# Kernel tuning notes

Hardware: AMD Instinct MI355X
Metric: run time of the kernel (lower is better)

## Reference

```python
import jax, jax.numpy as jnp
import numpy as np

D = 1024
E = 8


def setup_inputs() -> dict:
    key = jax.random.key(0)
    ks = jax.random.split(key, 7)
    s = 1.0 / np.sqrt(D)
    x = jax.random.normal(ks[0], (4, 2048, D), dtype=jnp.float32)
    Wg = jax.random.uniform(ks[1], (D, E), minval=-s, maxval=s, dtype=jnp.float32)
    bg = jax.random.uniform(ks[2], (E,), minval=-s, maxval=s, dtype=jnp.float32)
    W1 = jax.random.uniform(ks[3], (E, D, D), minval=-s, maxval=s, dtype=jnp.float32)
    b1 = jax.random.uniform(ks[4], (E, D), minval=-s, maxval=s, dtype=jnp.float32)
    W2 = jax.random.uniform(ks[5], (E, D, D), minval=-s, maxval=s, dtype=jnp.float32)
    b2 = jax.random.uniform(ks[6], (E, D), minval=-s, maxval=s, dtype=jnp.float32)
    return {"x": x, "Wg": Wg, "bg": bg, "W1": W1, "b1": b1, "W2": W2, "b2": b2}


def reference(x, Wg, bg, W1, b1, W2, b2):
    N, T, d = x.shape
    x_flat = x.reshape(N * T, d)                                  # [NT, D]
    logits = x_flat @ Wg + bg                                     # [NT, E]
    probs = jax.nn.softmax(logits, axis=-1)
    assignments = jnp.argmax(probs, axis=-1)                      # [NT]
    # all-experts MLP (dense, as in the original module)
    h = jnp.einsum('nd,edh->neh', x_flat, W1) + b1[None]          # [NT, E, D]
    h = jax.nn.gelu(h, approximate=False)                         # torch GELU = exact erf
    eo = jnp.einsum('neh,ehd->ned', h, W2) + b2[None]             # [NT, E, D]
    selected = jnp.take_along_axis(eo, assignments[:, None, None], axis=1)[:, 0, :]  # [NT, D]
    w = jnp.take_along_axis(probs, assignments[:, None], axis=1)  # [NT, 1]
    out = (w * selected).reshape(N, T, d)
    return out
```

## Files before the change

kernel.cpp:

```cpp
#include <hip/hip_runtime.h>
#include <cstdint>

#define NT 8192
#define DD 1024
#define NE 8
#define BK 32
#define NKIT (DD / BK)
#define TM 128
#define MAXTILE 72
#define TPX (MAXTILE / 8)

typedef __attribute__((ext_vector_type(8))) _Float16 half8;
typedef __attribute__((ext_vector_type(4))) float f32x4;

__device__ __forceinline__ unsigned short f2h_bits(float f) {
  _Float16 h = (_Float16)f;
  return __builtin_bit_cast(unsigned short, h);
}

#define GLDS16(gp, lp) __builtin_amdgcn_global_load_lds( \
  (__attribute__((address_space(1))) void*)(uintptr_t)(gp), \
  (__attribute__((address_space(3))) void*)(uintptr_t)(lp), 16, 0, 0)

#define WAITCNT_VM4  0xF74
#define WAITCNT_VM0  0xF70

__global__ __launch_bounds__(256) void prep_kernel(
    const float* __restrict__ W1, const float* __restrict__ W2,
    _Float16* __restrict__ W1t, _Float16* __restrict__ W2t,
    const float* __restrict__ x, const float* __restrict__ Wg, const float* __restrict__ bg,
    int* __restrict__ assign, float* __restrict__ wgt, _Float16* __restrict__ xh) {
  __shared__ alignas(16) char smem[32768];
  const int bid = blockIdx.x;
  const int tid = threadIdx.x;
  if (bid < 4096) {
    float (*tile)[65] = (float (*)[65])smem;
    const int z = bid >> 8;
    const float* W = (z < 8 ? W1 : W2) + (size_t)(z & 7) * (DD * DD);
    _Float16* Wt   = (z < 8 ? W1t : W2t) + (size_t)(z & 7) * (DD * DD);
    const int k0 = (bid & 15) * 64, n0 = ((bid >> 4) & 15) * 64;
#pragma unroll
    for (int it = 0; it < 4; ++it) {
      int idx = it * 256 + tid;
      int r = idx >> 4;
      int q = idx & 15;
      float4 v = *(const float4*)(W + (size_t)(k0 + r) * DD + n0 + q * 4);
      tile[r][q * 4 + 0] = v.x; tile[r][q * 4 + 1] = v.y;
      tile[r][q * 4 + 2] = v.z; tile[r][q * 4 + 3] = v.w;
    }
    __syncthreads();
#pragma unroll
    for (int it = 0; it < 4; ++it) {
      int idx = it * 256 + tid;
      int n = idx >> 4;
      int q = idx & 15;
      ushort4 o;
      o.x = f2h_bits(tile[q * 4 + 0][n]);
      o.y = f2h_bits(tile[q * 4 + 1][n]);
      o.z = f2h_bits(tile[q * 4 + 2][n]);
      o.w = f2h_bits(tile[q * 4 + 3][n]);
      *(ushort4*)(Wt + (size_t)(n0 + n) * DD + k0 + q * 4) = o;
    }
  } else {
    float* WgL = (float*)smem;
    const int gb = bid - 4096;
#pragma unroll
    for (int it = 0; it < 8; ++it) {
      int idx = it * 256 + tid;
      float4 v = ((const float4*)Wg)[idx];
      int k = idx >> 1;
      int e0 = (idx & 1) * 4;
      WgL[(e0 + 0) * DD + k] = v.x;
      WgL[(e0 + 1) * DD + k] = v.y;
      WgL[(e0 + 2) * DD + k] = v.z;
      WgL[(e0 + 3) * DD + k] = v.w;
    }
    __syncthreads();
    const int lane = tid & 63, w = tid >> 6;
#pragma unroll
    for (int s = 0; s < 2; ++s) {
      const int t = gb * 8 + w * 2 + s;
      const float4* xr = (const float4*)(x + (size_t)t * DD);
      float4 xv[4];
#pragma unroll
      for (int c = 0; c < 4; ++c) xv[c] = xr[lane + 64 * c];
      ushort4* xo = (ushort4*)(xh + (size_t)t * DD);
#pragma unroll
      for (int c = 0; c < 4; ++c) {
        union { ushort4 u; _Float16 h[4]; } cv;
        cv.h[0] = (_Float16)xv[c].x; cv.h[1] = (_Float16)xv[c].y;
        cv.h[2] = (_Float16)xv[c].z; cv.h[3] = (_Float16)xv[c].w;
        xo[lane + 64 * c] = cv.u;
      }
      float p[NE];
#pragma unroll
      for (int e = 0; e < NE; ++e) {
        float acc = 0.f;
#pragma unroll
        for (int c = 0; c < 4; ++c) {
          float4 wv = *(const float4*)&WgL[e * DD + 4 * lane + 256 * c];
          acc += xv[c].x * wv.x + xv[c].y * wv.y + xv[c].z * wv.z + xv[c].w * wv.w;
        }
        p[e] = acc;
      }
#pragma unroll
      for (int e = 0; e < NE; ++e) {
        float v = p[e];
        for (int off = 32; off > 0; off >>= 1) v += __shfl_down(v, off, 64);
        p[e] = v;
      }
      if (lane == 0) {
        float l[NE];
#pragma unroll
        for (int e = 0; e < NE; ++e) l[e] = p[e] + bg[e];
        int a = 0; float best = l[0];
#pragma unroll
        for (int e = 1; e < NE; ++e) if (l[e] > best) { best = l[e]; a = e; }
        float sum = 0.f;
#pragma unroll
        for (int e = 0; e < NE; ++e) sum += expf(l[e] - best);
        assign[t] = a;
        wgt[t] = 1.0f / sum;
      }
    }
  }
}

__global__ __launch_bounds__(1024) void sort_kernel(
    const int* __restrict__ assign, int* __restrict__ rowtok, int* __restrict__ plan) {
  __shared__ int wsum[16][NE];
  __shared__ int wbase[16][NE];
  __shared__ int s_offs[NE];
  __shared__ int s_tot[NE];
  __shared__ int s_pref[NE + 1];
  const int tid = threadIdx.x;
  const int lane = tid & 63, wv = tid >> 6;
  int a[8];
  int c[NE];
#pragma unroll
  for (int e = 0; e < NE; ++e) c[e] = 0;
#pragma unroll
  for (int j = 0; j < 8; ++j) { a[j] = assign[tid * 8 + j]; ++c[a[j]]; }
  int inc[NE];
#pragma unroll
  for (int e = 0; e < NE; ++e) inc[e] = c[e];
  for (int d = 1; d < 64; d <<= 1) {
#pragma unroll
    for (int e = 0; e < NE; ++e) {
      int u = __shfl_up(inc[e], d, 64);
      if (lane >= d) inc[e] += u;
    }
  }
  if (lane == 63) {
#pragma unroll
    for (int e = 0; e < NE; ++e) wsum[wv][e] = inc[e];
  }
  __syncthreads();
  if (wv == 0 && lane < 16) {
    int v[NE], incw[NE];
#pragma unroll
    for (int e = 0; e < NE; ++e) { v[e] = wsum[lane][e]; incw[e] = v[e]; }
    for (int d = 1; d < 16; d <<= 1) {
#pragma unroll
      for (int e = 0; e < NE; ++e) {
        int u = __shfl_up(incw[e], d, 64);
        if (lane >= d) incw[e] += u;
      }
    }
    int tote[NE];
#pragma unroll
    for (int e = 0; e < NE; ++e) tote[e] = __shfl(incw[e], 15, 64);
    int offs[NE];
    {
      int s = 0;
#pragma unroll
      for (int e = 0; e < NE; ++e) { offs[e] = s; s += tote[e]; }
    }
#pragma unroll
    for (int e = 0; e < NE; ++e) wbase[lane][e] = offs[e] + incw[e] - v[e];
    if (lane == 0) {
      int s = 0;
#pragma unroll
      for (int e = 0; e < NE; ++e) {
        s_offs[e] = offs[e]; s_tot[e] = tote[e];
        s_pref[e] = s; s += (tote[e] + TM - 1) / TM;
      }
      s_pref[NE] = s;
      plan[0] = s;
    }
  }
  __syncthreads();
  int run[NE];
#pragma unroll
  for (int e = 0; e < NE; ++e) run[e] = wbase[wv][e] + inc[e] - c[e];
#pragma unroll
  for (int j = 0; j < 8; ++j) { int e = a[j]; rowtok[run[e]++] = tid * 8 + j; }
  const int nt = s_pref[NE];
  if (tid < nt) {
    int e = 0;
    while (tid >= s_pref[e + 1]) ++e;
    int t = tid - s_pref[e];
    plan[1 + tid] = e;
    plan[1 + MAXTILE + tid] = s_offs[e] + t * TM;
    plan[1 + 2 * MAXTILE + tid] = s_offs[e] + s_tot[e];
  }
}

template <int MODE>
__global__ __launch_bounds__(256, 3) void gemm_kernel(
    const _Float16* __restrict__ A,
    const _Float16* __restrict__ Wt,
    const float* __restrict__ bias,
    const int* __restrict__ plan,
    _Float16* __restrict__ Hout,
    float* __restrict__ Fout,
    const int* __restrict__ rowtok,
    const float* __restrict__ wgt) {
  const int wrk = blockIdx.x;
  const int g = wrk & 7;
  const int r = wrk >> 3;
  const int tile = g * TPX + (r >> 3);
  const int nb = r & 7;
  if (tile >= plan[0]) return;
  const int e = plan[1 + tile];
  const int m0 = plan[1 + MAXTILE + tile];
  const int seg_end = plan[1 + 2 * MAXTILE + tile];
  const int n0 = nb * 128;

  const int tid = threadIdx.x;
  const int lane = tid & 63;
  const int wv = tid >> 6;
  const int wm = wv >> 1;
  const int wq = wv & 1;
  const int quad = lane >> 4;
  const int r15 = lane & 15;

  __shared__ alignas(16) char lds[49152];

  const _Float16* We = Wt + (size_t)e * DD * DD;
  const _Float16* gAp[2];
  const _Float16* gBp[2];
  int ldsoA[2], ldsoB[2];
#pragma unroll
  for (int i = 0; i < 2; ++i) {
    int slot = i * 256 + tid;
    int row = slot >> 2;
    int c = (slot & 3) ^ ((row >> 1) & 3);
    int rg = m0 + row; if (rg > NT - 1) rg = NT - 1;
    int arow = (MODE == 0) ? rowtok[rg] : rg;
    gAp[i] = A + (size_t)arow * DD + c * 8;
    ldsoA[i] = slot * 16;
    gBp[i] = We + (size_t)(n0 + row) * DD + c * 8;
    ldsoB[i] = slot * 16;
  }

  int aoff[4], boff[4];
#pragma unroll
  for (int i = 0; i < 4; ++i) {
    int m = wm * 64 + i * 16 + r15;
    aoff[i] = m * 4 + (quad ^ ((m >> 1) & 3));
    int n = wq * 64 + i * 16 + r15;
    boff[i] = n * 4 + (quad ^ ((n >> 1) & 3));
  }

  f32x4 acc[4][4];
  f32x4 zero4 = {0.f, 0.f, 0.f, 0.f};
#pragma unroll
  for (int mi = 0; mi < 4; ++mi)
#pragma unroll
    for (int ni = 0; ni < 4; ++ni) acc[mi][ni] = zero4;

#define LDSBUF(B) (lds + (B) * 16384)
#define STAGE(KT, BUF) do {                                          \
    const int ko_ = (KT) * BK;                                       \
    char* lb_ = LDSBUF(BUF);                                         \
    GLDS16(gAp[0] + ko_, lb_ + ldsoA[0]);                            \
    GLDS16(gAp[1] + ko_, lb_ + ldsoA[1]);                            \
    GLDS16(gBp[0] + ko_, lb_ + 8192 + ldsoB[0]);                     \
    GLDS16(gBp[1] + ko_, lb_ + 8192 + ldsoB[1]);                     \
  } while (0)
#define COMPUTE(BUF) do {                                            \
    const half8* AsV = (const half8*)(LDSBUF(BUF));                  \
    const half8* BsV = (const half8*)(LDSBUF(BUF) + 8192);           \
    half8 a_[4], b_[4];                                              \
    _Pragma("unroll")                                                \
    for (int i = 0; i < 4; ++i) a_[i] = AsV[aoff[i]];                \
    _Pragma("unroll")                                                \
    for (int i = 0; i < 4; ++i) b_[i] = BsV[boff[i]];                \
    _Pragma("unroll")                                                \
    for (int mi = 0; mi < 4; ++mi)                                   \
      _Pragma("unroll")                                              \
      for (int ni = 0; ni < 4; ++ni)                                 \
        acc[mi][ni] = __builtin_amdgcn_mfma_f32_16x16x32_f16(a_[mi], b_[ni], acc[mi][ni], 0, 0, 0); \
  } while (0)

  STAGE(0, 0);
  STAGE(1, 1);

#pragma unroll 1
  for (int kt = 0; kt < NKIT - 2; kt += 3) {
    __builtin_amdgcn_s_waitcnt(WAITCNT_VM4);
    __builtin_amdgcn_s_barrier();
    __asm__ volatile("" ::: "memory");
    STAGE(kt + 2, 2);
    COMPUTE(0);
    __builtin_amdgcn_s_waitcnt(WAITCNT_VM4);
    __builtin_amdgcn_s_barrier();
    __asm__ volatile("" ::: "memory");
    STAGE(kt + 3, 0);
    COMPUTE(1);
    __builtin_amdgcn_s_waitcnt(WAITCNT_VM4);
    __builtin_amdgcn_s_barrier();
    __asm__ volatile("" ::: "memory");
    STAGE(kt + 4, 1);
    COMPUTE(2);
  }
  __builtin_amdgcn_s_waitcnt(WAITCNT_VM4);
  __builtin_amdgcn_s_barrier();
  __asm__ volatile("" ::: "memory");
  COMPUTE(0);
  __builtin_amdgcn_s_waitcnt(WAITCNT_VM0);
  __builtin_amdgcn_s_barrier();
  __asm__ volatile("" ::: "memory");
  COMPUTE(1);
#undef COMPUTE
#undef STAGE
#undef LDSBUF

  const float* bptr = bias + (size_t)e * DD;
#pragma unroll
  for (int mi = 0; mi < 4; ++mi) {
    int rowb = m0 + wm * 64 + mi * 16 + quad * 4;
#pragma unroll
    for (int rr = 0; rr < 4; ++rr) {
      int gpos = rowb + rr;
      if (gpos < seg_end) {
        if (MODE == 0) {
#pragma unroll
          for (int ni = 0; ni < 4; ++ni) {
            int n = n0 + wq * 64 + ni * 16 + r15;
            float val = acc[mi][ni][rr] + bptr[n];
            val = 0.5f * val * (1.0f + erff(val * 0.70710678118654752f));
            Hout[(size_t)gpos * DD + n] = (_Float16)val;
          }
        } else {
          int tok = rowtok[gpos];
          float wgl = wgt[tok];
          float* orow = Fout + (size_t)tok * DD;
#pragma unroll
          for (int ni = 0; ni < 4; ++ni) {
            int n = n0 + wq * 64 + ni * 16 + r15;
            orow[n] = (acc[mi][ni][rr] + bptr[n]) * wgl;
          }
        }
      }
    }
  }
}

extern "C" void kernel_launch(void* const* d_in, const int* in_sizes, int n_in,
                              void* d_out, int out_size, void* d_ws, size_t ws_size,
                              hipStream_t stream) {
  const float* x  = (const float*)d_in[0];
  const float* Wg = (const float*)d_in[1];
  const float* bg = (const float*)d_in[2];
  const float* W1 = (const float*)d_in[3];
  const float* b1 = (const float*)d_in[4];
  const float* W2 = (const float*)d_in[5];
  const float* b2 = (const float*)d_in[6];
  float* out = (float*)d_out;

  char* ws = (char*)d_ws;
  const size_t MB16 = (size_t)1 << 24;
  _Float16* W1t = (_Float16*)(ws + 0 * MB16);
  _Float16* W2t = (_Float16*)(ws + 1 * MB16);
  _Float16* xh  = (_Float16*)(ws + 2 * MB16);
  _Float16* H   = (_Float16*)(ws + 3 * MB16);
  int*   assign = (int*)(ws + 4 * MB16);
  int*   rowtok = assign + NT;
  float* wgt    = (float*)(rowtok + NT);
  int*   plan   = (int*)(wgt + NT);

  prep_kernel<<<4096 + NT / 8, 256, 0, stream>>>(W1, W2, W1t, W2t, x, Wg, bg, assign, wgt, xh);
  sort_kernel<<<1, 1024, 0, stream>>>(assign, rowtok, plan);
  gemm_kernel<0><<<MAXTILE * 8, 256, 0, stream>>>(xh, W1t, b1, plan, H, nullptr, rowtok, nullptr);
  gemm_kernel<1><<<MAXTILE * 8, 256, 0, stream>>>(H, W2t, b2, plan, nullptr, out, rowtok, wgt);
}
```

Baseline: 229.2 us.

## Fuse prep, sort and both expert GEMMs into one persistent kernel with grid barriers

Replaces four kernel launches with a single persistent kernel of 576 blocks that runs the phases in order, separated by atomic grid barriers. The W2 fp16 cast is moved into the same phase as the single-block token sort, so the sort no longer serializes the GPU. The sort is rewritten for 256 threads with 32 tokens per thread. This removes launch gaps and the idle sort kernel, but relies on all 576 blocks being co-resident (3 per CU) and adds the cost of the barrier spin-waits.

Result: slower. 761.3 us (+232.2%).

```diff
diff --git a/kernel.cpp b/kernel.cpp
--- a/kernel.cpp
+++ b/kernel.cpp
@@ -9,6 +9,7 @@
 #define TM 128
 #define MAXTILE 72
 #define TPX (MAXTILE / 8)
+#define GRID 576
 
 typedef __attribute__((ext_vector_type(8))) _Float16 half8;
 typedef __attribute__((ext_vector_type(4))) float f32x4;
@@ -25,122 +26,125 @@
 #define WAITCNT_VM4  0xF74
 #define WAITCNT_VM0  0xF70
 
-__global__ __launch_bounds__(256) void prep_kernel(
-    const float* __restrict__ W1, const float* __restrict__ W2,
-    _Float16* __restrict__ W1t, _Float16* __restrict__ W2t,
-    const float* __restrict__ x, const float* __restrict__ Wg, const float* __restrict__ bg,
-    int* __restrict__ assign, float* __restrict__ wgt, _Float16* __restrict__ xh) {
-  __shared__ alignas(16) char smem[32768];
-  const int bid = blockIdx.x;
-  const int tid = threadIdx.x;
-  if (bid < 4096) {
-    float (*tile)[65] = (float (*)[65])smem;
-    const int z = bid >> 8;
-    const float* W = (z < 8 ? W1 : W2) + (size_t)(z & 7) * (DD * DD);
-    _Float16* Wt   = (z < 8 ? W1t : W2t) + (size_t)(z & 7) * (DD * DD);
-    const int k0 = (bid & 15) * 64, n0 = ((bid >> 4) & 15) * 64;
-#pragma unroll
-    for (int it = 0; it < 4; ++it) {
-      int idx = it * 256 + tid;
-      int r = idx >> 4;
-      int q = idx & 15;
-      float4 v = *(const float4*)(W + (size_t)(k0 + r) * DD + n0 + q * 4);
-      tile[r][q * 4 + 0] = v.x; tile[r][q * 4 + 1] = v.y;
-      tile[r][q * 4 + 2] = v.z; tile[r][q * 4 + 3] = v.w;
-    }
-    __syncthreads();
-#pragma unroll
-    for (int it = 0; it < 4; ++it) {
-      int idx = it * 256 + tid;
-      int n = idx >> 4;
-      int q = idx & 15;
-      ushort4 o;
-      o.x = f2h_bits(tile[q * 4 + 0][n]);
-      o.y = f2h_bits(tile[q * 4 + 1][n]);
-      o.z = f2h_bits(tile[q * 4 + 2][n]);
-      o.w = f2h_bits(tile[q * 4 + 3][n]);
-      *(ushort4*)(Wt + (size_t)(n0 + n) * DD + k0 + q * 4) = o;
-    }
-  } else {
-    float* WgL = (float*)smem;
-    const int gb = bid - 4096;
-#pragma unroll
-    for (int it = 0; it < 8; ++it) {
-      int idx = it * 256 + tid;
-      float4 v = ((const float4*)Wg)[idx];
-      int k = idx >> 1;
-      int e0 = (idx & 1) * 4;
-      WgL[(e0 + 0) * DD + k] = v.x;
-      WgL[(e0 + 1) * DD + k] = v.y;
-      WgL[(e0 + 2) * DD + k] = v.z;
-      WgL[(e0 + 3) * DD + k] = v.w;
-    }
-    __syncthreads();
-    const int lane = tid & 63, w = tid >> 6;
-#pragma unroll
-    for (int s = 0; s < 2; ++s) {
-      const int t = gb * 8 + w * 2 + s;
-      const float4* xr = (const float4*)(x + (size_t)t * DD);
-      float4 xv[4];
-#pragma unroll
-      for (int c = 0; c < 4; ++c) xv[c] = xr[lane + 64 * c];
-      ushort4* xo = (ushort4*)(xh + (size_t)t * DD);
+__device__ __forceinline__ void gridbar(unsigned* bar, unsigned target) {
+  __threadfence();
+  __syncthreads();
+  if (threadIdx.x == 0) {
+    __hip_atomic_fetch_add(bar, 1u, __ATOMIC_ACQ_REL, __HIP_MEMORY_SCOPE_AGENT);
+    while (__hip_atomic_load(bar, __ATOMIC_RELAXED, __HIP_MEMORY_SCOPE_AGENT) < target) {
+      __builtin_amdgcn_s_sleep(2);
+    }
+  }
+  __syncthreads();
+  __threadfence();
+}
+
+__device__ void wcast_job(const float* __restrict__ W, _Float16* __restrict__ Wt,
+                          int j, int tid, char* smem) {
+  float (*tile)[65] = (float (*)[65])smem;
+  const float* Ws = W + (size_t)(j >> 8) * (DD * DD);
+  _Float16* Wd    = Wt + (size_t)(j >> 8) * (DD * DD);
+  const int k0 = ((j >> 4) & 15) * 64, n0 = (j & 15) * 64;
+#pragma unroll
+  for (int it = 0; it < 4; ++it) {
+    int idx = it * 256 + tid;
+    int r = idx >> 4;
+    int q = idx & 15;
+    float4 v = *(const float4*)(Ws + (size_t)(k0 + r) * DD + n0 + q * 4);
+    tile[r][q * 4 + 0] = v.x; tile[r][q * 4 + 1] = v.y;
+    tile[r][q * 4 + 2] = v.z; tile[r][q * 4 + 3] = v.w;
+  }
+  __syncthreads();
+#pragma unroll
+  for (int it = 0; it < 4; ++it) {
+    int idx = it * 256 + tid;
+    int n = idx >> 4;
+    int q = idx & 15;
+    ushort4 o;
+    o.x = f2h_bits(tile[q * 4 + 0][n]);
+    o.y = f2h_bits(tile[q * 4 + 1][n]);
+    o.z = f2h_bits(tile[q * 4 + 2][n]);
+    o.w = f2h_bits(tile[q * 4 + 3][n]);
+    *(ushort4*)(Wd + (size_t)(n0 + n) * DD + k0 + q * 4) = o;
+  }
+}
+
+__device__ void gate_job(const float* __restrict__ x, const float* __restrict__ Wg,
+                         const float* __restrict__ bg, int* __restrict__ assign,
+                         float* __restrict__ wgt, _Float16* __restrict__ xh,
+                         int j, int tid, char* smem) {
+  float* WgL = (float*)smem;
+#pragma unroll
+  for (int it = 0; it < 8; ++it) {
+    int idx = it * 256 + tid;
+    float4 v = ((const float4*)Wg)[idx];
+    int k = idx >> 1;
+    int e0 = (idx & 1) * 4;
+    WgL[(e0 + 0) * DD + k] = v.x;
+    WgL[(e0 + 1) * DD + k] = v.y;
+    WgL[(e0 + 2) * DD + k] = v.z;
+    WgL[(e0 + 3) * DD + k] = v.w;
+  }
+  __syncthreads();
+  const int lane = tid & 63, w = tid >> 6;
+#pragma unroll
+  for (int s = 0; s < 2; ++s) {
+    const int t = j * 8 + w * 2 + s;
+    const float4* xr = (const float4*)(x + (size_t)t * DD);
+    float4 xv[4];
+#pragma unroll
+    for (int c = 0; c < 4; ++c) xv[c] = xr[lane + 64 * c];
+    ushort4* xo = (ushort4*)(xh + (size_t)t * DD);
+#pragma unroll
+    for (int c = 0; c < 4; ++c) {
+      union { ushort4 u; _Float16 h[4]; } cv;
+      cv.h[0] = (_Float16)xv[c].x; cv.h[1] = (_Float16)xv[c].y;
+      cv.h[2] = (_Float16)xv[c].z; cv.h[3] = (_Float16)xv[c].w;
+      xo[lane + 64 * c] = cv.u;
+    }
+    float p[NE];
+#pragma unroll
+    for (int e = 0; e < NE; ++e) {
+      float acc = 0.f;
 #pragma unroll
       for (int c = 0; c < 4; ++c) {
-        union { ushort4 u; _Float16 h[4]; } cv;
-        cv.h[0] = (_Float16)xv[c].x; cv.h[1] = (_Float16)xv[c].y;
-        cv.h[2] = (_Float16)xv[c].z; cv.h[3] = (_Float16)xv[c].w;
-        xo[lane + 64 * c] = cv.u;
+        float4 wv = *(const float4*)&WgL[e * DD + 4 * lane + 256 * c];
+        acc += xv[c].x * wv.x + xv[c].y * wv.y + xv[c].z * wv.z + xv[c].w * wv.w;
       }
-      float p[NE];
-#pragma unroll
-      for (int e = 0; e < NE; ++e) {
-        float acc = 0.f;
-#pragma unroll
-        for (int c = 0; c < 4; ++c) {
-          float4 wv = *(const float4*)&WgL[e * DD + 4 * lane + 256 * c];
-          acc += xv[c].x * wv.x + xv[c].y * wv.y + xv[c].z * wv.z + xv[c].w * wv.w;
-        }
-        p[e] = acc;
-      }
-#pragma unroll
-      for (int e = 0; e < NE; ++e) {
-        float v = p[e];
-        for (int off = 32; off > 0; off >>= 1) v += __shfl_down(v, off, 64);
-        p[e] = v;
-      }
-      if (lane == 0) {
-        float l[NE];
-#pragma unroll
-        for (int e = 0; e < NE; ++e) l[e] = p[e] + bg[e];
-        int a = 0; float best = l[0];
-#pragma unroll
-        for (int e = 1; e < NE; ++e) if (l[e] > best) { best = l[e]; a = e; }
-        float sum = 0.f;
-#pragma unroll
-        for (int e = 0; e < NE; ++e) sum += expf(l[e] - best);
-        assign[t] = a;
-        wgt[t] = 1.0f / sum;
-      }
-    }
-  }
-}
-
-__global__ __launch_bounds__(1024) void sort_kernel(
-    const int* __restrict__ assign, int* __restrict__ rowtok, int* __restrict__ plan) {
-  __shared__ int wsum[16][NE];
-  __shared__ int wbase[16][NE];
-  __shared__ int s_offs[NE];
-  __shared__ int s_tot[NE];
-  __shared__ int s_pref[NE + 1];
-  const int tid = threadIdx.x;
+      p[e] = acc;
+    }
+#pragma unroll
+    for (int e = 0; e < NE; ++e) {
+      float v = p[e];
+      for (int off = 32; off > 0; off >>= 1) v += __shfl_down(v, off, 64);
+      p[e] = v;
+    }
+    if (lane == 0) {
+      float l[NE];
+#pragma unroll
+      for (int e = 0; e < NE; ++e) l[e] = p[e] + bg[e];
+      int a = 0; float best = l[0];
+#pragma unroll
+      for (int e = 1; e < NE; ++e) if (l[e] > best) { best = l[e]; a = e; }
+      float sum = 0.f;
+#pragma unroll
+      for (int e = 0; e < NE; ++e) sum += expf(l[e] - best);
+      assign[t] = a;
+      wgt[t] = 1.0f / sum;
+    }
+  }
+}
+
+__device__ void sort_256(const int* __restrict__ assign, int* __restrict__ rowtok,
+                         int* __restrict__ plan, int tid, char* smem) {
+  int (*wsum)[NE] = (int (*)[NE])smem;
   const int lane = tid & 63, wv = tid >> 6;
-  int a[8];
+  int a[32];
   int c[NE];
 #pragma unroll
   for (int e = 0; e < NE; ++e) c[e] = 0;
 #pragma unroll
-  for (int j = 0; j < 8; ++j) { a[j] = assign[tid * 8 + j]; ++c[a[j]]; }
+  for (int j = 0; j < 32; ++j) { a[j] = assign[tid * 32 + j]; ++c[a[j]]; }
   int inc[NE];
 #pragma unroll
   for (int e = 0; e < NE; ++e) inc[e] = c[e];
@@ -156,67 +160,49 @@
     for (int e = 0; e < NE; ++e) wsum[wv][e] = inc[e];
   }
   __syncthreads();
-  if (wv == 0 && lane < 16) {
-    int v[NE], incw[NE];
-#pragma unroll
-    for (int e = 0; e < NE; ++e) { v[e] = wsum[lane][e]; incw[e] = v[e]; }
-    for (int d = 1; d < 16; d <<= 1) {
-#pragma unroll
-      for (int e = 0; e < NE; ++e) {
-        int u = __shfl_up(incw[e], d, 64);
-        if (lane >= d) incw[e] += u;
-      }
-    }
-    int tote[NE];
-#pragma unroll
-    for (int e = 0; e < NE; ++e) tote[e] = __shfl(incw[e], 15, 64);
-    int offs[NE];
-    {
-      int s = 0;
-#pragma unroll
-      for (int e = 0; e < NE; ++e) { offs[e] = s; s += tote[e]; }
-    }
-#pragma unroll
-    for (int e = 0; e < NE; ++e) wbase[lane][e] = offs[e] + incw[e] - v[e];
-    if (lane == 0) {
-      int s = 0;
-#pragma unroll
-      for (int e = 0; e < NE; ++e) {
-        s_offs[e] = offs[e]; s_tot[e] = tote[e];
-        s_pref[e] = s; s += (tote[e] + TM - 1) / TM;
-      }
-      s_pref[NE] = s;
-      plan[0] = s;
-    }
-  }
-  __syncthreads();
+  int wb[NE], tote[NE];
+#pragma unroll
+  for (int e = 0; e < NE; ++e) {
+    int s = 0, t = 0;
+#pragma unroll
+    for (int w = 0; w < 4; ++w) { int v = wsum[w][e]; if (w < wv) s += v; t += v; }
+    wb[e] = s; tote[e] = t;
+  }
+  int offs[NE];
+  {
+    int s = 0;
+#pragma unroll
+    for (int e = 0; e < NE; ++e) { offs[e] = s; s += tote[e]; }
+  }
   int run[NE];
 #pragma unroll
-  for (int e = 0; e < NE; ++e) run[e] = wbase[wv][e] + inc[e] - c[e];
-#pragma unroll
-  for (int j = 0; j < 8; ++j) { int e = a[j]; rowtok[run[e]++] = tid * 8 + j; }
-  const int nt = s_pref[NE];
-  if (tid < nt) {
+  for (int e = 0; e < NE; ++e) run[e] = offs[e] + wb[e] + inc[e] - c[e];
+#pragma unroll
+  for (int j = 0; j < 32; ++j) { int e = a[j]; rowtok[run[e]++] = tid * 32 + j; }
+  int pref[NE + 1];
+  {
+    int s = 0;
+#pragma unroll
+    for (int e = 0; e < NE; ++e) { pref[e] = s; s += (tote[e] + TM - 1) / TM; }
+    pref[NE] = s;
+  }
+  if (tid == 0) plan[0] = pref[NE];
+  if (tid < pref[NE]) {
     int e = 0;
-    while (tid >= s_pref[e + 1]) ++e;
-    int t = tid - s_pref[e];
+    while (tid >= pref[e + 1]) ++e;
+    int t = tid - pref[e];
     plan[1 + tid] = e;
-    plan[1 + MAXTILE + tid] = s_offs[e] + t * TM;
-    plan[1 + 2 * MAXTILE + tid] = s_offs[e] + s_tot[e];
+    plan[1 + MAXTILE + tid] = offs[e] + t * TM;
+    plan[1 + 2 * MAXTILE + tid] = offs[e] + tote[e];
   }
 }
 
 template <int MODE>
-__global__ __launch_bounds__(256, 3) void gemm_kernel(
-    const _Float16* __restrict__ A,
-    const _Float16* __restrict__ Wt,
-    const float* __restrict__ bias,
-    const int* __restrict__ plan,
-    _Float16* __restrict__ Hout,
-    float* __restrict__ Fout,
-    const int* __restrict__ rowtok,
-    const float* __restrict__ wgt) {
-  const int wrk = blockIdx.x;
+__device__ void gemm_phase(int wrk,
+    const _Float16* __restrict__ A, const _Float16* __restrict__ Wt,
+    const float* __restrict__ bias, const int* __restrict__ plan,
+    _Float16* __restrict__ Hout, float* __restrict__ Fout,
+    const int* __restrict__ rowtok, const float* __restrict__ wgt, char* lds) {
   const int g = wrk & 7;
   const int r = wrk >> 3;
   const int tile = g * TPX + (r >> 3);
@@ -234,8 +220,6 @@
   const int wq = wv & 1;
   const int quad = lane >> 4;
   const int r15 = lane & 15;
-
-  __shared__ alignas(16) char lds[49152];
 
   const _Float16* We = Wt + (size_t)e * DD * DD;
   const _Float16* gAp[2];
@@ -358,6 +342,42 @@
   }
 }
 
+__global__ __launch_bounds__(256, 3) void fused_kernel(
+    const float* __restrict__ x, const float* __restrict__ Wg, const float* __restrict__ bg,
+    const float* __restrict__ W1, const float* __restrict__ b1,
+    const float* __restrict__ W2, const float* __restrict__ b2,
+    float* __restrict__ out,
+    _Float16* __restrict__ W1t, _Float16* __restrict__ W2t,
+    _Float16* __restrict__ xh, _Float16* __restrict__ H,
+    int* __restrict__ assign, int* __restrict__ rowtok,
+    float* __restrict__ wgt, int* __restrict__ plan, unsigned* __restrict__ bars) {
+  __shared__ alignas(16) char smem[49152];
+  const int bid = blockIdx.x;
+  const int tid = threadIdx.x;
+
+  for (int j = bid; j < 3072; j += GRID) {
+    if (j < 1024) gate_job(x, Wg, bg, assign, wgt, xh, j, tid, smem);
+    else          wcast_job(W1, W1t, j - 1024, tid, smem);
+    __syncthreads();
+  }
+  gridbar(bars + 0, GRID);
+
+  if (bid == 0) {
+    sort_256(assign, rowtok, plan, tid, smem);
+  } else {
+    for (int j = bid - 1; j < 2048; j += GRID - 1) {
+      wcast_job(W2, W2t, j, tid, smem);
+      __syncthreads();
+    }
+  }
+  gridbar(bars + 1, GRID);
+
+  gemm_phase<0>(bid, xh, W1t, b1, plan, H, nullptr, rowtok, nullptr, smem);
+  gridbar(bars + 2, GRID);
+
+  gemm_phase<1>(bid, H, W2t, b2, plan, nullptr, out, rowtok, wgt, smem);
+}
+
 extern "C" void kernel_launch(void* const* d_in, const int* in_sizes, int n_in,
                               void* d_out, int out_size, void* d_ws, size_t ws_size,
                               hipStream_t stream) {
@@ -380,9 +400,9 @@
   int*   rowtok = assign + NT;
   float* wgt    = (float*)(rowtok + NT);
   int*   plan   = (int*)(wgt + NT);
-
-  prep_kernel<<<4096 + NT / 8, 256, 0, stream>>>(W1, W2, W1t, W2t, x, Wg, bg, assign, wgt, xh);
-  sort_kernel<<<1, 1024, 0, stream>>>(assign, rowtok, plan);
-  gemm_kernel<0><<<MAXTILE * 8, 256, 0, stream>>>(xh, W1t, b1, plan, H, nullptr, rowtok, nullptr);
-  gemm_kernel<1><<<MAXTILE * 8, 256, 0, stream>>>(H, W2t, b2, plan, nullptr, out, rowtok, wgt);
-}
+  unsigned* bars = (unsigned*)(plan + 512);
+
+  hipMemsetAsync(bars, 0, 64, stream);
+  fused_kernel<<<GRID, 256, 0, stream>>>(x, Wg, bg, W1, b1, W2, b2, out,
+                                         W1t, W2t, xh, H, assign, rowtok, wgt, plan, bars);
+}
```

## Fuse token sort into GEMM kernels, computing per-block routing redundantly in LDS

Applied to the files above, without the earlier changes.

Removes the single-block sort kernel and its launch. Each GEMM block now reads all 8192 assignments, runs a per-expert prefix scan across its 256 threads, derives its own tile/expert/segment, and scatters only the token ids for its 128-row tile into LDS. This cuts one serial kernel launch and the global rowtok/plan round trip. In exchange every block repeats the scan (32 assignment loads per thread, plus shuffles) and uses extra LDS and registers, which may reduce occupancy.

Result: slower. 272.1 us (+18.7%).

```diff
diff --git a/kernel.cpp b/kernel.cpp
--- a/kernel.cpp
+++ b/kernel.cpp
@@ -126,118 +126,100 @@
   }
 }
 
-__global__ __launch_bounds__(1024) void sort_kernel(
-    const int* __restrict__ assign, int* __restrict__ rowtok, int* __restrict__ plan) {
-  __shared__ int wsum[16][NE];
-  __shared__ int wbase[16][NE];
-  __shared__ int s_offs[NE];
-  __shared__ int s_tot[NE];
-  __shared__ int s_pref[NE + 1];
-  const int tid = threadIdx.x;
-  const int lane = tid & 63, wv = tid >> 6;
-  int a[8];
-  int c[NE];
-#pragma unroll
-  for (int e = 0; e < NE; ++e) c[e] = 0;
-#pragma unroll
-  for (int j = 0; j < 8; ++j) { a[j] = assign[tid * 8 + j]; ++c[a[j]]; }
-  int inc[NE];
-#pragma unroll
-  for (int e = 0; e < NE; ++e) inc[e] = c[e];
-  for (int d = 1; d < 64; d <<= 1) {
-#pragma unroll
-    for (int e = 0; e < NE; ++e) {
-      int u = __shfl_up(inc[e], d, 64);
-      if (lane >= d) inc[e] += u;
-    }
-  }
-  if (lane == 63) {
-#pragma unroll
-    for (int e = 0; e < NE; ++e) wsum[wv][e] = inc[e];
-  }
-  __syncthreads();
-  if (wv == 0 && lane < 16) {
-    int v[NE], incw[NE];
-#pragma unroll
-    for (int e = 0; e < NE; ++e) { v[e] = wsum[lane][e]; incw[e] = v[e]; }
-    for (int d = 1; d < 16; d <<= 1) {
-#pragma unroll
-      for (int e = 0; e < NE; ++e) {
-        int u = __shfl_up(incw[e], d, 64);
-        if (lane >= d) incw[e] += u;
-      }
-    }
-    int tote[NE];
-#pragma unroll
-    for (int e = 0; e < NE; ++e) tote[e] = __shfl(incw[e], 15, 64);
-    int offs[NE];
-    {
-      int s = 0;
-#pragma unroll
-      for (int e = 0; e < NE; ++e) { offs[e] = s; s += tote[e]; }
-    }
-#pragma unroll
-    for (int e = 0; e < NE; ++e) wbase[lane][e] = offs[e] + incw[e] - v[e];
-    if (lane == 0) {
-      int s = 0;
-#pragma unroll
-      for (int e = 0; e < NE; ++e) {
-        s_offs[e] = offs[e]; s_tot[e] = tote[e];
-        s_pref[e] = s; s += (tote[e] + TM - 1) / TM;
-      }
-      s_pref[NE] = s;
-      plan[0] = s;
-    }
-  }
-  __syncthreads();
-  int run[NE];
-#pragma unroll
-  for (int e = 0; e < NE; ++e) run[e] = wbase[wv][e] + inc[e] - c[e];
-#pragma unroll
-  for (int j = 0; j < 8; ++j) { int e = a[j]; rowtok[run[e]++] = tid * 8 + j; }
-  const int nt = s_pref[NE];
-  if (tid < nt) {
-    int e = 0;
-    while (tid >= s_pref[e + 1]) ++e;
-    int t = tid - s_pref[e];
-    plan[1 + tid] = e;
-    plan[1 + MAXTILE + tid] = s_offs[e] + t * TM;
-    plan[1 + 2 * MAXTILE + tid] = s_offs[e] + s_tot[e];
-  }
-}
-
 template <int MODE>
 __global__ __launch_bounds__(256, 3) void gemm_kernel(
     const _Float16* __restrict__ A,
     const _Float16* __restrict__ Wt,
     const float* __restrict__ bias,
-    const int* __restrict__ plan,
+    const int* __restrict__ assign,
     _Float16* __restrict__ Hout,
     float* __restrict__ Fout,
-    const int* __restrict__ rowtok,
     const float* __restrict__ wgt) {
+  __shared__ alignas(16) char lds[50176];
+  int* rowtok_lds = (int*)(lds + 49152);
+  int (*wsum)[NE] = (int (*)[NE])(lds + 49152 + TM * 4);
+
+  const int tid = threadIdx.x;
+  const int lane = tid & 63;
+  const int wv = tid >> 6;
+
+  int at[32];
+  int c[NE];
+#pragma unroll
+  for (int e = 0; e < NE; ++e) c[e] = 0;
+#pragma unroll
+  for (int j = 0; j < 32; ++j) { at[j] = assign[tid * 32 + j]; ++c[at[j]]; }
+  int inc[NE];
+#pragma unroll
+  for (int e = 0; e < NE; ++e) inc[e] = c[e];
+  for (int d = 1; d < 64; d <<= 1) {
+#pragma unroll
+    for (int e = 0; e < NE; ++e) {
+      int u = __shfl_up(inc[e], d, 64);
+      if (lane >= d) inc[e] += u;
+    }
+  }
+  if (lane == 63) {
+#pragma unroll
+    for (int e = 0; e < NE; ++e) wsum[wv][e] = inc[e];
+  }
+  if (tid < TM) rowtok_lds[tid] = 0;
+  __syncthreads();
+  int wb[NE], tote[NE];
+#pragma unroll
+  for (int e = 0; e < NE; ++e) {
+    int s = 0, t = 0;
+#pragma unroll
+    for (int w = 0; w < 4; ++w) { int v = wsum[w][e]; if (w < wv) s += v; t += v; }
+    wb[e] = s; tote[e] = t;
+  }
+  int offs[NE];
+  {
+    int s = 0;
+#pragma unroll
+    for (int e = 0; e < NE; ++e) { offs[e] = s; s += tote[e]; }
+  }
+  int pref[NE + 1];
+  {
+    int s = 0;
+#pragma unroll
+    for (int e = 0; e < NE; ++e) { pref[e] = s; s += (tote[e] + TM - 1) / TM; }
+    pref[NE] = s;
+  }
+
   const int wrk = blockIdx.x;
   const int g = wrk & 7;
   const int r = wrk >> 3;
   const int tile = g * TPX + (r >> 3);
   const int nb = r & 7;
-  if (tile >= plan[0]) return;
-  const int e = plan[1 + tile];
-  const int m0 = plan[1 + MAXTILE + tile];
-  const int seg_end = plan[1 + 2 * MAXTILE + tile];
+  if (tile >= pref[NE]) return;
+  int eid = 0;
+#pragma unroll
+  for (int e = 0; e < NE; ++e) if (tile >= pref[e + 1]) eid = e + 1;
+  const int m0 = offs[eid] + (tile - pref[eid]) * TM;
+  const int seg_end = offs[eid] + tote[eid];
   const int n0 = nb * 128;
 
-  const int tid = threadIdx.x;
-  const int lane = tid & 63;
-  const int wv = tid >> 6;
+  {
+    int run[NE];
+#pragma unroll
+    for (int e = 0; e < NE; ++e) run[e] = offs[e] + wb[e] + inc[e] - c[e];
+#pragma unroll
+    for (int j = 0; j < 32; ++j) {
+      int e = at[j];
+      int p = run[e]++;
+      int rel = p - m0;
+      if ((unsigned)rel < (unsigned)TM) rowtok_lds[rel] = tid * 32 + j;
+    }
+  }
+  __syncthreads();
+
   const int wm = wv >> 1;
   const int wq = wv & 1;
   const int quad = lane >> 4;
   const int r15 = lane & 15;
 
-  __shared__ alignas(16) char lds[49152];
-
-  const _Float16* We = Wt + (size_t)e * DD * DD;
+  const _Float16* We = Wt + (size_t)eid * DD * DD;
   const _Float16* gAp[2];
   const _Float16* gBp[2];
   int ldsoA[2], ldsoB[2];
@@ -245,12 +227,17 @@
   for (int i = 0; i < 2; ++i) {
     int slot = i * 256 + tid;
     int row = slot >> 2;
-    int c = (slot & 3) ^ ((row >> 1) & 3);
-    int rg = m0 + row; if (rg > NT - 1) rg = NT - 1;
-    int arow = (MODE == 0) ? rowtok[rg] : rg;
-    gAp[i] = A + (size_t)arow * DD + c * 8;
+    int cc = (slot & 3) ^ ((row >> 1) & 3);
+    int arow;
+    if (MODE == 0) {
+      arow = rowtok_lds[row];
+    } else {
+      int rg = m0 + row; if (rg > NT - 1) rg = NT - 1;
+      arow = rg;
+    }
+    gAp[i] = A + (size_t)arow * DD + cc * 8;
     ldsoA[i] = slot * 16;
-    gBp[i] = We + (size_t)(n0 + row) * DD + c * 8;
+    gBp[i] = We + (size_t)(n0 + row) * DD + cc * 8;
     ldsoB[i] = slot * 16;
   }
 
@@ -327,7 +314,7 @@
 #undef STAGE
 #undef LDSBUF
 
-  const float* bptr = bias + (size_t)e * DD;
+  const float* bptr = bias + (size_t)eid * DD;
 #pragma unroll
   for (int mi = 0; mi < 4; ++mi) {
     int rowb = m0 + wm * 64 + mi * 16 + quad * 4;
@@ -344,7 +331,7 @@
             Hout[(size_t)gpos * DD + n] = (_Float16)val;
           }
         } else {
-          int tok = rowtok[gpos];
+          int tok = rowtok_lds[gpos - m0];
           float wgl = wgt[tok];
           float* orow = Fout + (size_t)tok * DD;
 #pragma unroll
@@ -377,12 +364,9 @@
   _Float16* xh  = (_Float16*)(ws + 2 * MB16);
   _Float16* H   = (_Float16*)(ws + 3 * MB16);
   int*   assign = (int*)(ws + 4 * MB16);
-  int*   rowtok = assign + NT;
-  float* wgt    = (float*)(rowtok + NT);
-  int*   plan   = (int*)(wgt + NT);
+  float* wgt    = (float*)(assign + NT);
 
   prep_kernel<<<4096 + NT / 8, 256, 0, stream>>>(W1, W2, W1t, W2t, x, Wg, bg, assign, wgt, xh);
-  sort_kernel<<<1, 1024, 0, stream>>>(assign, rowtok, plan);
-  gemm_kernel<0><<<MAXTILE * 8, 256, 0, stream>>>(xh, W1t, b1, plan, H, nullptr, rowtok, nullptr);
-  gemm_kernel<1><<<MAXTILE * 8, 256, 0, stream>>>(H, W2t, b2, plan, nullptr, out, rowtok, wgt);
+  gemm_kernel<0><<<MAXTILE * 8, 256, 0, stream>>>(xh, W1t, b1, assign, H, nullptr, wgt);
+  gemm_kernel<1><<<MAXTILE * 8, 256, 0, stream>>>(H, W2t, b2, assign, nullptr, out, wgt);
 }
```

## Fuse both expert GEMMs into one kernel with per-tile completion flags

Applied to the files above, without the earlier changes.

Merges the two expert GEMM launches into a single persistent-style kernel. Each block runs its first-layer slice, bumps an atomic per-tile counter, then spins until all eight N-blocks of that row tile have written H before running the second layer. This removes a kernel launch boundary and lets tiles start layer two without waiting for the whole first GEMM. In exchange it adds a memset and spin-waits, and it can deadlock if not all 576 blocks are co-resident. Occupancy is limited to 3 blocks per CU.

Result: slower. 264.6 us (+15.4%).

```diff
diff --git a/kernel.cpp b/kernel.cpp
--- a/kernel.cpp
+++ b/kernel.cpp
@@ -207,26 +207,11 @@
 }
 
 template <int MODE>
-__global__ __launch_bounds__(256, 3) void gemm_kernel(
-    const _Float16* __restrict__ A,
-    const _Float16* __restrict__ Wt,
-    const float* __restrict__ bias,
-    const int* __restrict__ plan,
-    _Float16* __restrict__ Hout,
-    float* __restrict__ Fout,
-    const int* __restrict__ rowtok,
-    const float* __restrict__ wgt) {
-  const int wrk = blockIdx.x;
-  const int g = wrk & 7;
-  const int r = wrk >> 3;
-  const int tile = g * TPX + (r >> 3);
-  const int nb = r & 7;
-  if (tile >= plan[0]) return;
-  const int e = plan[1 + tile];
-  const int m0 = plan[1 + MAXTILE + tile];
-  const int seg_end = plan[1 + 2 * MAXTILE + tile];
-  const int n0 = nb * 128;
-
+__device__ void gemm_body(
+    const _Float16* A, const _Float16* Wt, const float* bias,
+    _Float16* Hout, float* Fout,
+    const int* rowtok, const float* wgt, char* lds,
+    int e, int m0, int seg_end, int n0) {
   const int tid = threadIdx.x;
   const int lane = tid & 63;
   const int wv = tid >> 6;
@@ -234,8 +219,6 @@
   const int wq = wv & 1;
   const int quad = lane >> 4;
   const int r15 = lane & 15;
-
-  __shared__ alignas(16) char lds[49152];
 
   const _Float16* We = Wt + (size_t)e * DD * DD;
   const _Float16* gAp[2];
@@ -358,6 +341,41 @@
   }
 }
 
+__global__ __launch_bounds__(256, 3) void gemm_fused(
+    const _Float16* __restrict__ xh,
+    const _Float16* __restrict__ W1t, const float* __restrict__ b1,
+    _Float16* H,
+    const _Float16* __restrict__ W2t, const float* __restrict__ b2,
+    float* __restrict__ out,
+    const int* __restrict__ plan, const int* __restrict__ rowtok,
+    const float* __restrict__ wgt, unsigned* __restrict__ flags) {
+  __shared__ alignas(16) char lds[49152];
+  const int wrk = blockIdx.x;
+  const int g = wrk & 7;
+  const int r = wrk >> 3;
+  const int tile = g * TPX + (r >> 3);
+  const int nb = r & 7;
+  if (tile >= plan[0]) return;
+  const int e = plan[1 + tile];
+  const int m0 = plan[1 + MAXTILE + tile];
+  const int seg_end = plan[1 + 2 * MAXTILE + tile];
+  const int n0 = nb * 128;
+
+  gemm_body<0>(xh, W1t, b1, H, nullptr, rowtok, nullptr, lds, e, m0, seg_end, n0);
+
+  __syncthreads();
+  if (threadIdx.x == 0)
+    __hip_atomic_fetch_add(&flags[tile], 1u, __ATOMIC_RELEASE, __HIP_MEMORY_SCOPE_AGENT);
+
+  if (threadIdx.x == 0) {
+    while (__hip_atomic_load(&flags[tile], __ATOMIC_ACQUIRE, __HIP_MEMORY_SCOPE_AGENT) < 8u)
+      __builtin_amdgcn_s_sleep(2);
+  }
+  __syncthreads();
+
+  gemm_body<1>(H, W2t, b2, nullptr, out, rowtok, wgt, lds, e, m0, seg_end, n0);
+}
+
 extern "C" void kernel_launch(void* const* d_in, const int* in_sizes, int n_in,
                               void* d_out, int out_size, void* d_ws, size_t ws_size,
                               hipStream_t stream) {
@@ -380,9 +398,11 @@
   int*   rowtok = assign + NT;
   float* wgt    = (float*)(rowtok + NT);
   int*   plan   = (int*)(wgt + NT);
-
+  unsigned* flags = (unsigned*)(plan + 512);
+
+  hipMemsetAsync(flags, 0, MAXTILE * sizeof(unsigned), stream);
   prep_kernel<<<4096 + NT / 8, 256, 0, stream>>>(W1, W2, W1t, W2t, x, Wg, bg, assign, wgt, xh);
   sort_kernel<<<1, 1024, 0, stream>>>(assign, rowtok, plan);
-  gemm_kernel<0><<<MAXTILE * 8, 256, 0, stream>>>(xh, W1t, b1, plan, H, nullptr, rowtok, nullptr);
-  gemm_kernel<1><<<MAXTILE * 8, 256, 0, stream>>>(H, W2t, b2, plan, nullptr, out, rowtok, wgt);
-}
+  gemm_fused<<<MAXTILE * 8, 256, 0, stream>>>(xh, W1t, b1, H, W2t, b2, out,
+                                              plan, rowtok, wgt, flags);
+}
```
